# Performance work log

Hardware: AMD Instinct MI355X
Metric: run time of the kernel (lower is better)

The kernel has to match this reference:

```python
import jax, jax.numpy as jnp
import numpy as np

B, T, O, H, CTX, HOR = 32, 24, 128, 512, 256, 48
MAX_STEP = 2.0


def setup_inputs() -> dict:
    key = jax.random.key(0)
    ks = jax.random.split(key, 20)
    def lin(k, out_d, in_d):
        bound = 1.0 / np.sqrt(in_d)
        kw, kb = jax.random.split(k)
        W = jax.random.uniform(kw, (out_d, in_d), jnp.float32, -bound, bound)
        b = jax.random.uniform(kb, (out_d,), jnp.float32, -bound, bound)
        return W, b
    W_emb, b_emb = lin(ks[0], H, 2)
    W_ctx, b_ctx = lin(ks[1], H, CTX)
    Wi_enc, bi_enc = lin(ks[2], 3 * H, H)
    Wh_enc, bh_enc = lin(ks[3], 3 * H, H)
    Wi_cell, bi_cell = lin(ks[4], 3 * H, H)
    Wh_cell, bh_cell = lin(ks[5], 3 * H, H)
    W1, b1 = lin(ks[6], H, H)
    W2, b2 = lin(ks[7], 2, H)
    z_ctx = jax.random.normal(ks[8], (B, CTX), jnp.float32)
    traj_hist = jax.random.uniform(ks[9], (B, T, O, 2), jnp.float32) * 10.0
    return dict(z_ctx=z_ctx, traj_hist=traj_hist,
                W_emb=W_emb, b_emb=b_emb, W_ctx=W_ctx, b_ctx=b_ctx,
                Wi_enc=Wi_enc, Wh_enc=Wh_enc, bi_enc=bi_enc, bh_enc=bh_enc,
                Wi_cell=Wi_cell, Wh_cell=Wh_cell, bi_cell=bi_cell, bh_cell=bh_cell,
                W1=W1, b1=b1, W2=W2, b2=b2, horizon=HOR)


def _gru(h, x, Wi, Wh, bi, bh):
    # PyTorch GRU gate math: gates ordered (r, z, n)
    gi = x @ Wi.T + bi  # [N, 3H]
    gh = h @ Wh.T + bh
    ir, iz, inn = jnp.split(gi, 3, axis=-1)
    hr, hz, hn = jnp.split(gh, 3, axis=-1)
    r = jax.nn.sigmoid(ir + hr)
    z = jax.nn.sigmoid(iz + hz)
    n = jnp.tanh(inn + r * hn)
    return (1.0 - z) * n + z * h


def reference(z_ctx, traj_hist, W_emb, b_emb, W_ctx, b_ctx,
              Wi_enc, Wh_enc, bi_enc, bh_enc,
              Wi_cell, Wh_cell, bi_cell, bh_cell,
              W1, b1, W2, b2, horizon):
    b, t, o, _ = traj_hist.shape
    Hd = W_emb.shape[0]
    seq = traj_hist.transpose(0, 2, 1, 3).reshape(b * o, t, 2)  # [N, t, 2]
    emb = seq @ W_emb.T + b_emb  # [N, t, H]

    h0 = jnp.zeros((b * o, Hd), traj_hist.dtype)
    def enc_step(h, x):
        return _gru(h, x, Wi_enc, Wh_enc, bi_enc, bh_enc), None
    h, _ = jax.lax.scan(enc_step, h0, emb.transpose(1, 0, 2))

    ctx = z_ctx @ W_ctx.T + b_ctx                         # [b, H]
    ctx = jnp.repeat(ctx[:, None, :], o, axis=1).reshape(b * o, Hd)
    h = h + ctx

    state0 = seq[:, -1]  # [N, 2]
    def dec_step(carry, _):
        h, state = carry
        inp = state @ W_emb.T + b_emb
        h = _gru(h, inp, Wi_cell, Wh_cell, bi_cell, bh_cell)
        d = jax.nn.gelu(h @ W1.T + b1, approximate=False) @ W2.T + b2  # [N, 2]
        d = MAX_STEP * jnp.tanh(d / MAX_STEP)
        s = state + d
        state = jnp.stack([jnp.clip(s[..., 0], -90.0, 90.0),
                           jnp.mod(s[..., 1], 360.0)], axis=-1)
        return (h, state), state
    _, outs = jax.lax.scan(dec_step, (h, state0), None, length=horizon)
    # outs: [horizon, N, 2] -> [b, horizon, o, 2]
    return outs.transpose(1, 0, 2).reshape(b, o, horizon, 2).transpose(0, 2, 1, 3)
```

## Files before the change

kernel.cpp:

```cpp
#include <hip/hip_runtime.h>
#include <hip/hip_bf16.h>
#include <math.h>

#define BB 32
#define TT 24
#define OO 128
#define HH 512
#define CTXD 256
#define HOR 48
#define NN (BB*OO)
#define G3 (3*HH)
#define KS2 16
#define TILE_U16 (KS2*512)

typedef unsigned short ushortt;
typedef __attribute__((ext_vector_type(8))) short bf16x8;
typedef __attribute__((ext_vector_type(4))) float f32x4;

__device__ __forceinline__ ushortt f2bf(float x) {
    union { float f; unsigned u; } v; v.f = x;
    unsigned r = v.u + 0x7FFF + ((v.u >> 16) & 1);
    return (ushortt)(r >> 16);
}
__device__ __forceinline__ float bf2f(ushortt b) {
    union { unsigned u; float f; } v; v.u = ((unsigned)b) << 16;
    return v.f;
}
__device__ __forceinline__ void splitbf(float x, ushortt& hi, ushortt& lo) {
    hi = f2bf(x);
    lo = f2bf(x - bf2f(hi));
}
__device__ __forceinline__ float sigm(float x) { return 1.f / (1.f + __expf(-x)); }
__device__ __forceinline__ float tanh_fast(float x) {
    float xc = fminf(fmaxf(x, -10.f), 10.f);
    float e = __expf(2.f * xc);
    return (e - 1.f) / (e + 1.f);
}

__device__ __forceinline__ void group_barrier(unsigned* cnt, unsigned target) {
    __syncthreads();
    if (threadIdx.x == 0) {
        __hip_atomic_fetch_add(cnt, 1u, __ATOMIC_RELAXED, __HIP_MEMORY_SCOPE_AGENT);
        while (__hip_atomic_load(cnt, __ATOMIC_RELAXED, __HIP_MEMORY_SCOPE_AGENT) < target)
            __builtin_amdgcn_s_sleep(2);
    }
    __syncthreads();
    asm volatile("buffer_inv sc0\n\ts_waitcnt vmcnt(0)" ::: "memory");
}


#define MLOADA(Ad, ksv) do { const unsigned ko = (unsigned)(ksv) * 512; \
  _Pragma("unroll") for (int m_ = 0; m_ < 2; m_++) { \
    Ad[m_*2+0] = *reinterpret_cast<const bf16x8*>(RAh + ao[m_] + ko); \
    Ad[m_*2+1] = *reinterpret_cast<const bf16x8*>(RAl + ao[m_] + ko); \
  } } while(0)
#define MLOADB(Bd, ksv) do { const unsigned ko = (unsigned)(ksv) * 512; \
  _Pragma("unroll") for (int i_ = 0; i_ < 6; i_++) { \
    Bd[i_*2+0] = *reinterpret_cast<const bf16x8*>(Bh + bo[i_] + ko); \
    Bd[i_*2+1] = *reinterpret_cast<const bf16x8*>(Bl + bo[i_] + ko); \
  } } while(0)
#define MMFMA(Av, Bv) do { \
  _Pragma("unroll") for (int m_ = 0; m_ < 2; m_++) \
  _Pragma("unroll") for (int i_ = 0; i_ < 6; i_++) \
    acc[m_][i_] = __builtin_amdgcn_mfma_f32_16x16x32_bf16(Av[m_*2+0], Bv[i_*2+0], acc[m_][i_], 0,0,0); \
  _Pragma("unroll") for (int m_ = 0; m_ < 2; m_++) \
  _Pragma("unroll") for (int i_ = 0; i_ < 6; i_++) \
    acc[m_][i_] = __builtin_amdgcn_mfma_f32_16x16x32_bf16(Av[m_*2+0], Bv[i_*2+1], acc[m_][i_], 0,0,0); \
  _Pragma("unroll") for (int m_ = 0; m_ < 2; m_++) \
  _Pragma("unroll") for (int i_ = 0; i_ < 6; i_++) \
    acc[m_][i_] = __builtin_amdgcn_mfma_f32_16x16x32_bf16(Av[m_*2+1], Bv[i_*2+0], acc[m_][i_], 0,0,0); \
  } while(0)

#define HLOADA(Ad, ksv) do { const unsigned ko = (unsigned)(ksv) * 512; \
  _Pragma("unroll") for (int m_ = 0; m_ < 2; m_++) { \
    Ad[m_*2+0] = *reinterpret_cast<const bf16x8*>(WAh + ao[m_] + ko); \
    Ad[m_*2+1] = *reinterpret_cast<const bf16x8*>(WAl + ao[m_] + ko); \
  } } while(0)
#define HLOADB(Bd, ksv) do { const unsigned ko = (unsigned)(ksv) * 512; \
  _Pragma("unroll") for (int n_ = 0; n_ < 2; n_++) { \
    Bd[n_*2+0] = *reinterpret_cast<const bf16x8*>(W1H + bo1[n_] + ko); \
    Bd[n_*2+1] = *reinterpret_cast<const bf16x8*>(W1L + bo1[n_] + ko); \
  } } while(0)
#define HMFMA(Av, Bv) do { \
  _Pragma("unroll") for (int m_ = 0; m_ < 2; m_++) \
  _Pragma("unroll") for (int n_ = 0; n_ < 2; n_++) { \
    hacc[m_][n_] = __builtin_amdgcn_mfma_f32_16x16x32_bf16(Av[m_*2+0], Bv[n_*2+0], hacc[m_][n_], 0,0,0); \
    hacc[m_][n_] = __builtin_amdgcn_mfma_f32_16x16x32_bf16(Av[m_*2+0], Bv[n_*2+1], hacc[m_][n_], 0,0,0); \
    hacc[m_][n_] = __builtin_amdgcn_mfma_f32_16x16x32_bf16(Av[m_*2+1], Bv[n_*2+0], hacc[m_][n_], 0,0,0); \
  } } while(0)

__global__ __launch_bounds__(256, 2) void main_kernel(
    ushortt* Ah0, ushortt* Al0, ushortt* Ah1, ushortt* Al1,
    const ushortt* __restrict__ WheH, const ushortt* __restrict__ WheL,
    const ushortt* __restrict__ WhdH, const ushortt* __restrict__ WhdL,
    const ushortt* __restrict__ W1H,  const ushortt* __restrict__ W1L,
    const float* __restrict__ Ue, const float* __restrict__ ce,
    const float* __restrict__ Ud, const float* __restrict__ cd,
    const float* __restrict__ bhe, const float* __restrict__ bhd,
    const float* __restrict__ traj, const float* __restrict__ ctx,
    const float* __restrict__ b1v, const float* __restrict__ W2,
    const float* __restrict__ b2v, float* __restrict__ dpart,
    unsigned* bar, float* __restrict__ out)
{
    __shared__ float hbuf[128 * 36];
    __shared__ float sstate[128 * 2];
    const int mb = blockIdx.x & 31;
    const int jb = blockIdx.x >> 5;
    const int w = threadIdx.x >> 6, lane = threadIdx.x & 63;
    const int quad = lane >> 4, l15 = lane & 15;
    const int mtg = mb * 8 + w * 2;
    const int jlo = jb * 32;
    unsigned* grpcnt = bar + mb * 16;
    unsigned tgt = 0;

    ushortt* bh_[2] = {Ah0, Ah1};
    ushortt* bl_[2] = {Al0, Al1};

    unsigned ao[2], bo[6], bo1[2];
#pragma unroll
    for (int mt = 0; mt < 2; mt++) ao[mt] = (unsigned)(mtg + mt) * TILE_U16 + lane * 8;
#pragma unroll
    for (int g = 0; g < 3; g++)
#pragma unroll
        for (int jt = 0; jt < 2; jt++)
            bo[g*2+jt] = (unsigned)(g*32 + jb*2 + jt) * TILE_U16 + lane * 8;
#pragma unroll
    for (int nt = 0; nt < 2; nt++) bo1[nt] = (unsigned)(jb*2 + nt) * TILE_U16 + lane * 8;

    float b1r[2], w2a[2], w2b[2];
#pragma unroll
    for (int nt = 0; nt < 2; nt++) {
        int col = jlo + nt*16 + l15;
        b1r[nt] = b1v[col]; w2a[nt] = W2[col]; w2b[nt] = W2[HH + col];
    }
    const float b20 = b2v[0], b21 = b2v[1];

    float Ur0[2],Ur1[2],Uz0[2],Uz1[2],Un0[2],Un1[2],Crr[2],Czz[2],bhn[2],cinn[2];

#pragma unroll 1
    for (int s = 0; s < TT + HOR; s++) {
        const bool enc = s < TT;
        if (s == 0 || s == TT) {
            const float* U  = enc ? Ue : Ud;
            const float* ci = enc ? ce : cd;
            const float* bh = enc ? bhe : bhd;
#pragma unroll
            for (int jt = 0; jt < 2; jt++) {
                int j = jlo + jt*16 + l15;
                Ur0[jt] = U[j*2];            Ur1[jt] = U[j*2+1];
                Uz0[jt] = U[(512+j)*2];      Uz1[jt] = U[(512+j)*2+1];
                Un0[jt] = U[(1024+j)*2];     Un1[jt] = U[(1024+j)*2+1];
                Crr[jt] = ci[j] + bh[j];
                Czz[jt] = ci[512+j] + bh[512+j];
                cinn[jt] = ci[1024+j];       bhn[jt] = bh[1024+j];
            }
            if (!enc) {
                if (threadIdx.x < 128) {
                    int lrow = threadIdx.x;
                    const float* sp = traj + (((size_t)mb * TT + 23) * OO + lrow) * 2;
                    sstate[lrow*2] = sp[0]; sstate[lrow*2+1] = sp[1];
                }
                __syncthreads();
            }
        }
        const ushortt* RAh = bh_[s & 1];
        const ushortt* RAl = bl_[s & 1];
        ushortt* WAh = bh_[(s + 1) & 1];
        ushortt* WAl = bl_[(s + 1) & 1];
        const ushortt* Bh = enc ? WheH : WhdH;
        const ushortt* Bl = enc ? WheL : WhdL;

        f32x4 acc[2][6];
#pragma unroll
        for (int a = 0; a < 2; a++)
#pragma unroll
            for (int b = 0; b < 6; b++) acc[a][b] = (f32x4){0.f,0.f,0.f,0.f};

        if (s > 0) {
            bf16x8 aC[4], bC[12], aN[4], bN[12];
            MLOADA(aC, 0); MLOADB(bC, 0);
#pragma unroll 1
            for (int ks = 0; ks < 14; ks += 2) {
                MLOADA(aN, ks+1); MLOADB(bN, ks+1);
                MMFMA(aC, bC);
                MLOADA(aC, ks+2); MLOADB(bC, ks+2);
                MMFMA(aN, bN);
            }
            MLOADA(aN, 15); MLOADB(bN, 15);
            MMFMA(aC, bC);
            MMFMA(aN, bN);
        }

        float x0v[2][4], x1v[2][4];
#pragma unroll
        for (int mt = 0; mt < 2; mt++)
#pragma unroll
            for (int reg = 0; reg < 4; reg++) {
                int lrow = (w*2 + mt) * 16 + quad * 4 + reg;
                if (enc) {
                    const float* p = traj + (((size_t)mb * TT + s) * OO + lrow) * 2;
                    x0v[mt][reg] = p[0]; x1v[mt][reg] = p[1];
                } else {
                    x0v[mt][reg] = sstate[lrow*2]; x1v[mt][reg] = sstate[lrow*2+1];
                }
            }

#pragma unroll
        for (int mt = 0; mt < 2; mt++)
#pragma unroll
            for (int jt = 0; jt < 2; jt++) {
                int qk = jt*2 + (l15 >> 3), slot = l15 & 7;
#pragma unroll
                for (int reg = 0; reg < 4; reg++) {
                    float x0 = x0v[mt][reg], x1 = x1v[mt][reg];
                    float pr = acc[mt][0+jt][reg] + fmaf(x1, Ur1[jt], fmaf(x0, Ur0[jt], Crr[jt]));
                    float pz = acc[mt][2+jt][reg] + fmaf(x1, Uz1[jt], fmaf(x0, Uz0[jt], Czz[jt]));
                    float hn = acc[mt][4+jt][reg] + bhn[jt];
                    float inn = fmaf(x1, Un1[jt], fmaf(x0, Un0[jt], cinn[jt]));
                    float hold = 0.f;
                    if (s > 0) {
                        unsigned pos = (unsigned)(mtg + mt) * TILE_U16 + (unsigned)jb * 512
                                     + (unsigned)(qk*16 + quad*4 + reg) * 8 + slot;
                        hold = bf2f(RAh[pos]) + bf2f(RAl[pos]);
                    }
                    float rg = sigm(pr), zg = sigm(pz);
                    float nn = tanh_fast(inn + rg * hn);
                    float h = (1.f - zg) * nn + zg * hold;
                    if (enc && s == TT - 1)
                        h += ctx[(size_t)mb * HH + jlo + jt*16 + l15];
                    hbuf[(w*32 + mt*16 + quad*4 + reg) * 36 + jt*16 + l15] = h;
                }
            }
        __syncthreads();
#pragma unroll
        for (int rr = 0; rr < 2; rr++) {
            int fr = threadIdx.x + 256 * rr;
            int mt8 = fr >> 6, fl = fr & 63;
            int qk = fl >> 4, rloc = mt8 * 16 + (fl & 15);
            const float4 v0 = *reinterpret_cast<const float4*>(&hbuf[rloc * 36 + qk * 8]);
            const float4 v1 = *reinterpret_cast<const float4*>(&hbuf[rloc * 36 + qk * 8 + 4]);
            float src[8] = {v0.x, v0.y, v0.z, v0.w, v1.x, v1.y, v1.z, v1.w};
            bf16x8 hv, lv;
#pragma unroll
            for (int q = 0; q < 8; q++) {
                ushortt hi, lo; splitbf(src[q], hi, lo);
                hv[q] = (short)hi; lv[q] = (short)lo;
            }
            unsigned base = (unsigned)(mb*8 + mt8) * TILE_U16 + (unsigned)jb * 512 + fl * 8;
            *reinterpret_cast<bf16x8*>(WAh + base) = hv;
            *reinterpret_cast<bf16x8*>(WAl + base) = lv;
        }
        __syncthreads();

        tgt += 16;
        group_barrier(grpcnt, tgt);

        if (!enc) {
            f32x4 hacc[2][2];
#pragma unroll
            for (int a = 0; a < 2; a++)
#pragma unroll
                for (int b = 0; b < 2; b++) hacc[a][b] = (f32x4){0.f,0.f,0.f,0.f};
            {
                bf16x8 aC[4], bC[4], aN[4], bN[4];
                HLOADA(aC, 0); HLOADB(bC, 0);
#pragma unroll 1
                for (int ks = 0; ks < 14; ks += 2) {
                    HLOADA(aN, ks+1); HLOADB(bN, ks+1);
                    HMFMA(aC, bC);
                    HLOADA(aC, ks+2); HLOADB(bC, ks+2);
                    HMFMA(aN, bN);
                }
                HLOADA(aN, 15); HLOADB(bN, 15);
                HMFMA(aC, bC);
                HMFMA(aN, bN);
            }
            float p0[2][4], p1[2][4];
#pragma unroll
            for (int mt = 0; mt < 2; mt++)
#pragma unroll
                for (int reg = 0; reg < 4; reg++) { p0[mt][reg] = 0.f; p1[mt][reg] = 0.f; }
#pragma unroll
            for (int mt = 0; mt < 2; mt++)
#pragma unroll
                for (int nt = 0; nt < 2; nt++)
#pragma unroll
                    for (int reg = 0; reg < 4; reg++) {
                        float v = hacc[mt][nt][reg] + b1r[nt];
                        v = 0.5f * v * (1.0f + erff(v * 0.70710678118654752440f));
                        p0[mt][reg] = fmaf(v, w2a[nt], p0[mt][reg]);
                        p1[mt][reg] = fmaf(v, w2b[nt], p1[mt][reg]);
                    }
#pragma unroll
            for (int m = 1; m < 16; m <<= 1)
#pragma unroll
                for (int mt = 0; mt < 2; mt++)
#pragma unroll
                    for (int reg = 0; reg < 4; reg++) {
                        p0[mt][reg] += __shfl_xor(p0[mt][reg], m, 64);
                        p1[mt][reg] += __shfl_xor(p1[mt][reg], m, 64);
                    }
            if (l15 == 0) {
#pragma unroll
                for (int mt = 0; mt < 2; mt++)
#pragma unroll
                    for (int reg = 0; reg < 4; reg++) {
                        int lrow = (w*2 + mt) * 16 + quad * 4 + reg;
                        float* dp = dpart + ((size_t)(mb*16 + jb) * 128 + lrow) * 2;
                        dp[0] = p0[mt][reg]; dp[1] = p1[mt][reg];
                    }
            }
            tgt += 16;
            group_barrier(grpcnt, tgt);
            if (threadIdx.x < 128) {
                int lrow = threadIdx.x;
                float d0 = 0.f, d1 = 0.f;
#pragma unroll
                for (int j2 = 0; j2 < 16; j2++) {
                    const float* dp = dpart + ((size_t)(mb*16 + j2) * 128 + lrow) * 2;
                    d0 += dp[0]; d1 += dp[1];
                }
                d0 += b20; d1 += b21;
                d0 = 2.0f * tanhf(d0 * 0.5f);
                d1 = 2.0f * tanhf(d1 * 0.5f);
                float s0 = sstate[lrow*2] + d0;
                s0 = fminf(fmaxf(s0, -90.f), 90.f);
                float s1 = sstate[lrow*2+1] + d1;
                float rrm = fmodf(s1, 360.f);
                if (rrm < 0.f) rrm += 360.f;
                sstate[lrow*2] = s0; sstate[lrow*2+1] = rrm;
                if (jb == 0) {
                    float* op = out + (((size_t)mb * HOR + (s - TT)) * OO + lrow) * 2;
                    op[0] = s0; op[1] = rrm;
                }
            }
            __syncthreads();
        }
    }
}

__device__ __forceinline__ void pack16(const float* __restrict__ W,
                                       ushortt* __restrict__ Fh, ushortt* __restrict__ Fl,
                                       int item) {
    int n = item >> 6, rem = item & 63;
    int ks = rem >> 2, quadk = rem & 3;
    int nt = n >> 4, l15 = n & 15;
    ushortt hv[8], lv[8];
#pragma unroll
    for (int q = 0; q < 8; q++) {
        float v = W[(size_t)n * 512 + ks*32 + quadk*8 + q];
        ushortt hi, lo; splitbf(v, hi, lo);
        hv[q] = hi; lv[q] = lo;
    }
    size_t pos = ((size_t)nt * TILE_U16) + (size_t)ks * 512 + (quadk*16 + l15) * 8;
#pragma unroll
    for (int q = 0; q < 8; q++) { Fh[pos + q] = hv[q]; Fl[pos + q] = lv[q]; }
}

__global__ __launch_bounds__(256) void prep_kernel(
    const float* __restrict__ Wh_enc, const float* __restrict__ Wh_cell,
    const float* __restrict__ W1,
    const float* __restrict__ Wi_enc, const float* __restrict__ bi_enc,
    const float* __restrict__ Wi_cell, const float* __restrict__ bi_cell,
    const float* __restrict__ W_emb, const float* __restrict__ b_emb,
    const float* __restrict__ z, const float* __restrict__ Wc, const float* __restrict__ bc,
    ushortt* __restrict__ WheH, ushortt* __restrict__ WheL,
    ushortt* __restrict__ WhdH, ushortt* __restrict__ WhdL,
    ushortt* __restrict__ W1H, ushortt* __restrict__ W1L,
    float* __restrict__ Ue, float* __restrict__ ce,
    float* __restrict__ Ud, float* __restrict__ cd,
    float* __restrict__ ctx, unsigned* __restrict__ bar)
{
    int b = blockIdx.x;
    if (b < 384) {
        pack16(Wh_enc, WheH, WheL, b * 256 + threadIdx.x);
    } else if (b < 768) {
        pack16(Wh_cell, WhdH, WhdL, (b - 384) * 256 + threadIdx.x);
    } else if (b < 896) {
        pack16(W1, W1H, W1L, (b - 768) * 256 + threadIdx.x);
    } else if (b < 1664) {
        int w = threadIdx.x >> 6, lane = threadIdx.x & 63;
        int gidx = (b - 896) * 4 + w;
        int which = gidx >= G3;
        int j = gidx - which * G3;
        const float* Wi = which ? Wi_cell : Wi_enc;
        const float* bi = which ? bi_cell : bi_enc;
        float u0 = 0.f, u1 = 0.f, cc = 0.f;
#pragma unroll
        for (int i = 0; i < 8; i++) {
            int k = i * 64 + lane;
            float wv = Wi[(size_t)j * HH + k];
            u0 = fmaf(wv, W_emb[2*k],   u0);
            u1 = fmaf(wv, W_emb[2*k+1], u1);
            cc = fmaf(wv, b_emb[k],     cc);
        }
#pragma unroll
        for (int m = 1; m < 64; m <<= 1) {
            u0 += __shfl_xor(u0, m, 64);
            u1 += __shfl_xor(u1, m, 64);
            cc += __shfl_xor(cc, m, 64);
        }
        if (lane == 0) {
            float* Uo = which ? Ud : Ue;
            float* cv = which ? cd : ce;
            Uo[j*2] = u0; Uo[j*2+1] = u1; cv[j] = cc + bi[j];
        }
    } else if (b < 1728) {
        int idx = (b - 1664) * 256 + threadIdx.x;
        int bb = idx >> 9, j = idx & 511;
        float acc = bc[j];
        const float4* zp = (const float4*)(z + (size_t)bb * CTXD);
        const float4* wp = (const float4*)(Wc + (size_t)j * CTXD);
#pragma unroll 4
        for (int k = 0; k < CTXD / 4; k++) {
            float4 a = zp[k], ww = wp[k];
            acc = fmaf(a.x, ww.x, fmaf(a.y, ww.y, fmaf(a.z, ww.z, fmaf(a.w, ww.w, acc))));
        }
        ctx[idx] = acc;
    } else {
        bar[threadIdx.x] = 0u;
        bar[threadIdx.x + 256] = 0u;
    }
}

extern "C" void kernel_launch(void* const* d_in, const int* in_sizes, int n_in,
                              void* d_out, int out_size, void* d_ws, size_t ws_size,
                              hipStream_t stream) {
    const float* z_ctx   = (const float*)d_in[0];
    const float* traj    = (const float*)d_in[1];
    const float* W_emb   = (const float*)d_in[2];
    const float* b_emb   = (const float*)d_in[3];
    const float* W_ctx   = (const float*)d_in[4];
    const float* b_ctx   = (const float*)d_in[5];
    const float* Wi_enc  = (const float*)d_in[6];
    const float* Wh_enc  = (const float*)d_in[7];
    const float* bi_enc  = (const float*)d_in[8];
    const float* bh_enc  = (const float*)d_in[9];
    const float* Wi_cell = (const float*)d_in[10];
    const float* Wh_cell = (const float*)d_in[11];
    const float* bi_cell = (const float*)d_in[12];
    const float* bh_cell = (const float*)d_in[13];
    const float* W1      = (const float*)d_in[14];
    const float* b1      = (const float*)d_in[15];
    const float* W2      = (const float*)d_in[16];
    const float* b2      = (const float*)d_in[17];
    float* out = (float*)d_out;

    char* ws = (char*)d_ws;
    size_t off = 0;
    auto alloc = [&](size_t bytes) { void* p = ws + off; off += (bytes + 255) & ~(size_t)255; return p; };
    const size_t hfrag  = (size_t)256 * TILE_U16 * 2;
    const size_t wfrag  = (size_t)96  * TILE_U16 * 2;
    const size_t w1frag = (size_t)32  * TILE_U16 * 2;
    ushortt* Ah0 = (ushortt*)alloc(hfrag);
    ushortt* Al0 = (ushortt*)alloc(hfrag);
    ushortt* Ah1 = (ushortt*)alloc(hfrag);
    ushortt* Al1 = (ushortt*)alloc(hfrag);
    ushortt* WheH = (ushortt*)alloc(wfrag);
    ushortt* WheL = (ushortt*)alloc(wfrag);
    ushortt* WhdH = (ushortt*)alloc(wfrag);
    ushortt* WhdL = (ushortt*)alloc(wfrag);
    ushortt* W1H  = (ushortt*)alloc(w1frag);
    ushortt* W1L  = (ushortt*)alloc(w1frag);
    float*   Ue   = (float*)alloc((size_t)G3 * 2 * 4);
    float*   ce   = (float*)alloc((size_t)G3 * 4);
    float*   Ud   = (float*)alloc((size_t)G3 * 2 * 4);
    float*   cd   = (float*)alloc((size_t)G3 * 4);
    float*   ctxb = (float*)alloc((size_t)BB * HH * 4);
    float*   dpart = (float*)alloc((size_t)32 * 16 * 128 * 2 * 4);
    unsigned* bar  = (unsigned*)alloc(512 * 4);

    prep_kernel<<<1729, 256, 0, stream>>>(Wh_enc, Wh_cell, W1,
                                          Wi_enc, bi_enc, Wi_cell, bi_cell,
                                          W_emb, b_emb, z_ctx, W_ctx, b_ctx,
                                          WheH, WheL, WhdH, WhdL, W1H, W1L,
                                          Ue, ce, Ud, cd, ctxb, bar);

    main_kernel<<<512, 256, 0, stream>>>(Ah0, Al0, Ah1, Al1,
                                         WheH, WheL, WhdH, WhdL, W1H, W1L,
                                         Ue, ce, Ud, cd, bh_enc, bh_cell,
                                         traj, ctxb, b1, W2, b2,
                                         dpart, bar, out);
}
```

Before: 3.498 ms.

## Split hidden columns across twice as many blocks and keep old h in LDS

Each block now owns 16 hidden columns instead of 32, and the grid doubles to 1024 blocks with launch bounds raised to 4 blocks per CU. The per-block accumulators, B-fragment loads and W1 tiles shrink to match, and the partial sums for the output head are spread over 32 slices instead of 16. The previous hidden value is now read from the block's own LDS buffer rather than reloaded from the global split-bf16 buffers, and one __syncthreads before the group barrier is dropped. The aim is more parallelism and occupancy per step, at the price of a grid barrier that needs twice as many arrivals and more redundant A-operand loads across blocks.

```diff
diff --git a/kernel.cpp b/kernel.cpp
--- a/kernel.cpp
+++ b/kernel.cpp
@@ -55,20 +55,20 @@
     Ad[m_*2+1] = *reinterpret_cast<const bf16x8*>(RAl + ao[m_] + ko); \
   } } while(0)
 #define MLOADB(Bd, ksv) do { const unsigned ko = (unsigned)(ksv) * 512; \
-  _Pragma("unroll") for (int i_ = 0; i_ < 6; i_++) { \
-    Bd[i_*2+0] = *reinterpret_cast<const bf16x8*>(Bh + bo[i_] + ko); \
-    Bd[i_*2+1] = *reinterpret_cast<const bf16x8*>(Bl + bo[i_] + ko); \
+  _Pragma("unroll") for (int g_ = 0; g_ < 3; g_++) { \
+    Bd[g_*2+0] = *reinterpret_cast<const bf16x8*>(Bh + bo[g_] + ko); \
+    Bd[g_*2+1] = *reinterpret_cast<const bf16x8*>(Bl + bo[g_] + ko); \
   } } while(0)
 #define MMFMA(Av, Bv) do { \
   _Pragma("unroll") for (int m_ = 0; m_ < 2; m_++) \
-  _Pragma("unroll") for (int i_ = 0; i_ < 6; i_++) \
-    acc[m_][i_] = __builtin_amdgcn_mfma_f32_16x16x32_bf16(Av[m_*2+0], Bv[i_*2+0], acc[m_][i_], 0,0,0); \
+  _Pragma("unroll") for (int g_ = 0; g_ < 3; g_++) \
+    acc[m_][g_] = __builtin_amdgcn_mfma_f32_16x16x32_bf16(Av[m_*2+0], Bv[g_*2+0], acc[m_][g_], 0,0,0); \
   _Pragma("unroll") for (int m_ = 0; m_ < 2; m_++) \
-  _Pragma("unroll") for (int i_ = 0; i_ < 6; i_++) \
-    acc[m_][i_] = __builtin_amdgcn_mfma_f32_16x16x32_bf16(Av[m_*2+0], Bv[i_*2+1], acc[m_][i_], 0,0,0); \
+  _Pragma("unroll") for (int g_ = 0; g_ < 3; g_++) \
+    acc[m_][g_] = __builtin_amdgcn_mfma_f32_16x16x32_bf16(Av[m_*2+0], Bv[g_*2+1], acc[m_][g_], 0,0,0); \
   _Pragma("unroll") for (int m_ = 0; m_ < 2; m_++) \
-  _Pragma("unroll") for (int i_ = 0; i_ < 6; i_++) \
-    acc[m_][i_] = __builtin_amdgcn_mfma_f32_16x16x32_bf16(Av[m_*2+1], Bv[i_*2+0], acc[m_][i_], 0,0,0); \
+  _Pragma("unroll") for (int g_ = 0; g_ < 3; g_++) \
+    acc[m_][g_] = __builtin_amdgcn_mfma_f32_16x16x32_bf16(Av[m_*2+1], Bv[g_*2+0], acc[m_][g_], 0,0,0); \
   } while(0)
 
 #define HLOADA(Ad, ksv) do { const unsigned ko = (unsigned)(ksv) * 512; \
@@ -77,19 +77,17 @@
     Ad[m_*2+1] = *reinterpret_cast<const bf16x8*>(WAl + ao[m_] + ko); \
   } } while(0)
 #define HLOADB(Bd, ksv) do { const unsigned ko = (unsigned)(ksv) * 512; \
-  _Pragma("unroll") for (int n_ = 0; n_ < 2; n_++) { \
-    Bd[n_*2+0] = *reinterpret_cast<const bf16x8*>(W1H + bo1[n_] + ko); \
-    Bd[n_*2+1] = *reinterpret_cast<const bf16x8*>(W1L + bo1[n_] + ko); \
+    Bd[0] = *reinterpret_cast<const bf16x8*>(W1H + bo1 + ko); \
+    Bd[1] = *reinterpret_cast<const bf16x8*>(W1L + bo1 + ko); \
+  } while(0)
+#define HMFMA(Av, Bv) do { \
+  _Pragma("unroll") for (int m_ = 0; m_ < 2; m_++) { \
+    hacc[m_] = __builtin_amdgcn_mfma_f32_16x16x32_bf16(Av[m_*2+0], Bv[0], hacc[m_], 0,0,0); \
+    hacc[m_] = __builtin_amdgcn_mfma_f32_16x16x32_bf16(Av[m_*2+0], Bv[1], hacc[m_], 0,0,0); \
+    hacc[m_] = __builtin_amdgcn_mfma_f32_16x16x32_bf16(Av[m_*2+1], Bv[0], hacc[m_], 0,0,0); \
   } } while(0)
-#define HMFMA(Av, Bv) do { \
-  _Pragma("unroll") for (int m_ = 0; m_ < 2; m_++) \
-  _Pragma("unroll") for (int n_ = 0; n_ < 2; n_++) { \
-    hacc[m_][n_] = __builtin_amdgcn_mfma_f32_16x16x32_bf16(Av[m_*2+0], Bv[n_*2+0], hacc[m_][n_], 0,0,0); \
-    hacc[m_][n_] = __builtin_amdgcn_mfma_f32_16x16x32_bf16(Av[m_*2+0], Bv[n_*2+1], hacc[m_][n_], 0,0,0); \
-    hacc[m_][n_] = __builtin_amdgcn_mfma_f32_16x16x32_bf16(Av[m_*2+1], Bv[n_*2+0], hacc[m_][n_], 0,0,0); \
-  } } while(0)
-
-__global__ __launch_bounds__(256, 2) void main_kernel(
+
+__global__ __launch_bounds__(256, 4) void main_kernel(
     ushortt* Ah0, ushortt* Al0, ushortt* Ah1, ushortt* Al1,
     const ushortt* __restrict__ WheH, const ushortt* __restrict__ WheL,
     const ushortt* __restrict__ WhdH, const ushortt* __restrict__ WhdL,
@@ -102,40 +100,32 @@
     const float* __restrict__ b2v, float* __restrict__ dpart,
     unsigned* bar, float* __restrict__ out)
 {
-    __shared__ float hbuf[128 * 36];
+    __shared__ float hbuf[128 * 20];
     __shared__ float sstate[128 * 2];
     const int mb = blockIdx.x & 31;
     const int jb = blockIdx.x >> 5;
     const int w = threadIdx.x >> 6, lane = threadIdx.x & 63;
     const int quad = lane >> 4, l15 = lane & 15;
     const int mtg = mb * 8 + w * 2;
-    const int jlo = jb * 32;
+    const int jlo = jb * 16;
+    const int jcol = jlo + l15;
     unsigned* grpcnt = bar + mb * 16;
     unsigned tgt = 0;
 
     ushortt* bh_[2] = {Ah0, Ah1};
     ushortt* bl_[2] = {Al0, Al1};
 
-    unsigned ao[2], bo[6], bo1[2];
+    unsigned ao[2], bo[3], bo1;
 #pragma unroll
     for (int mt = 0; mt < 2; mt++) ao[mt] = (unsigned)(mtg + mt) * TILE_U16 + lane * 8;
 #pragma unroll
-    for (int g = 0; g < 3; g++)
-#pragma unroll
-        for (int jt = 0; jt < 2; jt++)
-            bo[g*2+jt] = (unsigned)(g*32 + jb*2 + jt) * TILE_U16 + lane * 8;
-#pragma unroll
-    for (int nt = 0; nt < 2; nt++) bo1[nt] = (unsigned)(jb*2 + nt) * TILE_U16 + lane * 8;
-
-    float b1r[2], w2a[2], w2b[2];
-#pragma unroll
-    for (int nt = 0; nt < 2; nt++) {
-        int col = jlo + nt*16 + l15;
-        b1r[nt] = b1v[col]; w2a[nt] = W2[col]; w2b[nt] = W2[HH + col];
-    }
+    for (int g = 0; g < 3; g++) bo[g] = (unsigned)(g*32 + jb) * TILE_U16 + lane * 8;
+    bo1 = (unsigned)jb * TILE_U16 + lane * 8;
+
+    const float b1r = b1v[jcol], w2a = W2[jcol], w2b = W2[HH + jcol];
     const float b20 = b2v[0], b21 = b2v[1];
 
-    float Ur0[2],Ur1[2],Uz0[2],Uz1[2],Un0[2],Un1[2],Crr[2],Czz[2],bhn[2],cinn[2];
+    float Ur0, Ur1, Uz0, Uz1, Un0, Un1, Crr, Czz, bhn, cinn;
 
 #pragma unroll 1
     for (int s = 0; s < TT + HOR; s++) {
@@ -144,16 +134,12 @@
             const float* U  = enc ? Ue : Ud;
             const float* ci = enc ? ce : cd;
             const float* bh = enc ? bhe : bhd;
-#pragma unroll
-            for (int jt = 0; jt < 2; jt++) {
-                int j = jlo + jt*16 + l15;
-                Ur0[jt] = U[j*2];            Ur1[jt] = U[j*2+1];
-                Uz0[jt] = U[(512+j)*2];      Uz1[jt] = U[(512+j)*2+1];
-                Un0[jt] = U[(1024+j)*2];     Un1[jt] = U[(1024+j)*2+1];
-                Crr[jt] = ci[j] + bh[j];
-                Czz[jt] = ci[512+j] + bh[512+j];
-                cinn[jt] = ci[1024+j];       bhn[jt] = bh[1024+j];
-            }
+            Ur0 = U[jcol*2];            Ur1 = U[jcol*2+1];
+            Uz0 = U[(512+jcol)*2];      Uz1 = U[(512+jcol)*2+1];
+            Un0 = U[(1024+jcol)*2];     Un1 = U[(1024+jcol)*2+1];
+            Crr = ci[jcol] + bh[jcol];
+            Czz = ci[512+jcol] + bh[512+jcol];
+            cinn = ci[1024+jcol];       bhn = bh[1024+jcol];
             if (!enc) {
                 if (threadIdx.x < 128) {
                     int lrow = threadIdx.x;
@@ -170,14 +156,14 @@
         const ushortt* Bh = enc ? WheH : WhdH;
         const ushortt* Bl = enc ? WheL : WhdL;
 
-        f32x4 acc[2][6];
+        f32x4 acc[2][3];
 #pragma unroll
         for (int a = 0; a < 2; a++)
 #pragma unroll
-            for (int b = 0; b < 6; b++) acc[a][b] = (f32x4){0.f,0.f,0.f,0.f};
+            for (int g = 0; g < 3; g++) acc[a][g] = (f32x4){0.f,0.f,0.f,0.f};
 
         if (s > 0) {
-            bf16x8 aC[4], bC[12], aN[4], bN[12];
+            bf16x8 aC[4], bC[6], aN[4], bN[6];
             MLOADA(aC, 0); MLOADB(bC, 0);
 #pragma unroll 1
             for (int ks = 0; ks < 14; ks += 2) {
@@ -208,37 +194,28 @@
 #pragma unroll
         for (int mt = 0; mt < 2; mt++)
 #pragma unroll
-            for (int jt = 0; jt < 2; jt++) {
-                int qk = jt*2 + (l15 >> 3), slot = l15 & 7;
-#pragma unroll
-                for (int reg = 0; reg < 4; reg++) {
-                    float x0 = x0v[mt][reg], x1 = x1v[mt][reg];
-                    float pr = acc[mt][0+jt][reg] + fmaf(x1, Ur1[jt], fmaf(x0, Ur0[jt], Crr[jt]));
-                    float pz = acc[mt][2+jt][reg] + fmaf(x1, Uz1[jt], fmaf(x0, Uz0[jt], Czz[jt]));
-                    float hn = acc[mt][4+jt][reg] + bhn[jt];
-                    float inn = fmaf(x1, Un1[jt], fmaf(x0, Un0[jt], cinn[jt]));
-                    float hold = 0.f;
-                    if (s > 0) {
-                        unsigned pos = (unsigned)(mtg + mt) * TILE_U16 + (unsigned)jb * 512
-                                     + (unsigned)(qk*16 + quad*4 + reg) * 8 + slot;
-                        hold = bf2f(RAh[pos]) + bf2f(RAl[pos]);
-                    }
-                    float rg = sigm(pr), zg = sigm(pz);
-                    float nn = tanh_fast(inn + rg * hn);
-                    float h = (1.f - zg) * nn + zg * hold;
-                    if (enc && s == TT - 1)
-                        h += ctx[(size_t)mb * HH + jlo + jt*16 + l15];
-                    hbuf[(w*32 + mt*16 + quad*4 + reg) * 36 + jt*16 + l15] = h;
-                }
+            for (int reg = 0; reg < 4; reg++) {
+                int lrow = (w*2 + mt) * 16 + quad * 4 + reg;
+                float x0 = x0v[mt][reg], x1 = x1v[mt][reg];
+                float pr = acc[mt][0][reg] + fmaf(x1, Ur1, fmaf(x0, Ur0, Crr));
+                float pz = acc[mt][1][reg] + fmaf(x1, Uz1, fmaf(x0, Uz0, Czz));
+                float hn = acc[mt][2][reg] + bhn;
+                float inn = fmaf(x1, Un1, fmaf(x0, Un0, cinn));
+                float hold = (s > 0) ? hbuf[lrow * 20 + l15] : 0.f;
+                float rg = sigm(pr), zg = sigm(pz);
+                float nn = tanh_fast(inn + rg * hn);
+                float h = (1.f - zg) * nn + zg * hold;
+                if (enc && s == TT - 1)
+                    h += ctx[(size_t)mb * HH + jcol];
+                hbuf[lrow * 20 + l15] = h;
             }
         __syncthreads();
-#pragma unroll
-        for (int rr = 0; rr < 2; rr++) {
-            int fr = threadIdx.x + 256 * rr;
-            int mt8 = fr >> 6, fl = fr & 63;
-            int qk = fl >> 4, rloc = mt8 * 16 + (fl & 15);
-            const float4 v0 = *reinterpret_cast<const float4*>(&hbuf[rloc * 36 + qk * 8]);
-            const float4 v1 = *reinterpret_cast<const float4*>(&hbuf[rloc * 36 + qk * 8 + 4]);
+        {
+            int fr = threadIdx.x;
+            int mt8 = fr >> 5, rem = fr & 31;
+            int qk = rem >> 4, r15 = rem & 15;
+            const float4 v0 = *reinterpret_cast<const float4*>(&hbuf[(mt8*16 + r15) * 20 + qk * 8]);
+            const float4 v1 = *reinterpret_cast<const float4*>(&hbuf[(mt8*16 + r15) * 20 + qk * 8 + 4]);
             float src[8] = {v0.x, v0.y, v0.z, v0.w, v1.x, v1.y, v1.z, v1.w};
             bf16x8 hv, lv;
 #pragma unroll
@@ -246,23 +223,22 @@
                 ushortt hi, lo; splitbf(src[q], hi, lo);
                 hv[q] = (short)hi; lv[q] = (short)lo;
             }
-            unsigned base = (unsigned)(mb*8 + mt8) * TILE_U16 + (unsigned)jb * 512 + fl * 8;
+            int quadg = (jb & 1) * 2 + qk;
+            unsigned base = (unsigned)(mb*8 + mt8) * TILE_U16 + (unsigned)(jb >> 1) * 512
+                          + (unsigned)(quadg * 16 + r15) * 8;
             *reinterpret_cast<bf16x8*>(WAh + base) = hv;
             *reinterpret_cast<bf16x8*>(WAl + base) = lv;
         }
-        __syncthreads();
-
-        tgt += 16;
+
+        tgt += 32;
         group_barrier(grpcnt, tgt);
 
         if (!enc) {
-            f32x4 hacc[2][2];
-#pragma unroll
-            for (int a = 0; a < 2; a++)
-#pragma unroll
-                for (int b = 0; b < 2; b++) hacc[a][b] = (f32x4){0.f,0.f,0.f,0.f};
+            f32x4 hacc[2];
+            hacc[0] = (f32x4){0.f,0.f,0.f,0.f};
+            hacc[1] = (f32x4){0.f,0.f,0.f,0.f};
             {
-                bf16x8 aC[4], bC[4], aN[4], bN[4];
+                bf16x8 aC[4], bC[2], aN[4], bN[2];
                 HLOADA(aC, 0); HLOADB(bC, 0);
 #pragma unroll 1
                 for (int ks = 0; ks < 14; ks += 2) {
@@ -279,18 +255,12 @@
 #pragma unroll
             for (int mt = 0; mt < 2; mt++)
 #pragma unroll
-                for (int reg = 0; reg < 4; reg++) { p0[mt][reg] = 0.f; p1[mt][reg] = 0.f; }
-#pragma unroll
-            for (int mt = 0; mt < 2; mt++)
-#pragma unroll
-                for (int nt = 0; nt < 2; nt++)
-#pragma unroll
-                    for (int reg = 0; reg < 4; reg++) {
-                        float v = hacc[mt][nt][reg] + b1r[nt];
-                        v = 0.5f * v * (1.0f + erff(v * 0.70710678118654752440f));
-                        p0[mt][reg] = fmaf(v, w2a[nt], p0[mt][reg]);
-                        p1[mt][reg] = fmaf(v, w2b[nt], p1[mt][reg]);
-                    }
+                for (int reg = 0; reg < 4; reg++) {
+                    float v = hacc[mt][reg] + b1r;
+                    v = 0.5f * v * (1.0f + erff(v * 0.70710678118654752440f));
+                    p0[mt][reg] = v * w2a;
+                    p1[mt][reg] = v * w2b;
+                }
 #pragma unroll
             for (int m = 1; m < 16; m <<= 1)
 #pragma unroll
@@ -306,18 +276,18 @@
 #pragma unroll
                     for (int reg = 0; reg < 4; reg++) {
                         int lrow = (w*2 + mt) * 16 + quad * 4 + reg;
-                        float* dp = dpart + ((size_t)(mb*16 + jb) * 128 + lrow) * 2;
+                        float* dp = dpart + ((size_t)(mb*32 + jb) * 128 + lrow) * 2;
                         dp[0] = p0[mt][reg]; dp[1] = p1[mt][reg];
                     }
             }
-            tgt += 16;
+            tgt += 32;
             group_barrier(grpcnt, tgt);
             if (threadIdx.x < 128) {
                 int lrow = threadIdx.x;
                 float d0 = 0.f, d1 = 0.f;
-#pragma unroll
-                for (int j2 = 0; j2 < 16; j2++) {
-                    const float* dp = dpart + ((size_t)(mb*16 + j2) * 128 + lrow) * 2;
+#pragma unroll 8
+                for (int j2 = 0; j2 < 32; j2++) {
+                    const float* dp = dpart + ((size_t)(mb*32 + j2) * 128 + lrow) * 2;
                     d0 += dp[0]; d1 += dp[1];
                 }
                 d0 += b20; d1 += b21;
@@ -462,13 +432,13 @@
     ushortt* WhdL = (ushortt*)alloc(wfrag);
     ushortt* W1H  = (ushortt*)alloc(w1frag);
     ushortt* W1L  = (ushortt*)alloc(w1frag);
-    float*   Ue   = (float*)alloc((size_t)G3 * 2 * 4);
-    float*   ce   = (float*)alloc((size_t)G3 * 4);
-    float*   Ud   = (float*)alloc((size_t)G3 * 2 * 4);
-    float*   cd   = (float*)alloc((size_t)G3 * 4);
-    float*   ctxb = (float*)alloc((size_t)BB * HH * 4);
-    float*   dpart = (float*)alloc((size_t)32 * 16 * 128 * 2 * 4);
-    unsigned* bar  = (unsigned*)alloc(512 * 4);
+    float* Ue   = (float*)alloc((size_t)G3 * 2 * 4);
+    float* ce   = (float*)alloc((size_t)G3 * 4);
+    float* Ud   = (float*)alloc((size_t)G3 * 2 * 4);
+    float* cd   = (float*)alloc((size_t)G3 * 4);
+    float* ctxb = (float*)alloc((size_t)BB * HH * 4);
+    float* dpart = (float*)alloc((size_t)32 * 32 * 128 * 2 * 4);
+    unsigned* bar = (unsigned*)alloc(512 * 4);
 
     prep_kernel<<<1729, 256, 0, stream>>>(Wh_enc, Wh_cell, W1,
                                           Wi_enc, bi_enc, Wi_cell, bi_cell,
@@ -476,9 +446,9 @@
                                           WheH, WheL, WhdH, WhdL, W1H, W1L,
                                           Ue, ce, Ud, cd, ctxb, bar);
 
-    main_kernel<<<512, 256, 0, stream>>>(Ah0, Al0, Ah1, Al1,
-                                         WheH, WheL, WhdH, WhdL, W1H, W1L,
-                                         Ue, ce, Ud, cd, bh_enc, bh_cell,
-                                         traj, ctxb, b1, W2, b2,
-                                         dpart, bar, out);
-}
+    main_kernel<<<1024, 256, 0, stream>>>(Ah0, Al0, Ah1, Al1,
+                                          WheH, WheL, WhdH, WhdL, W1H, W1L,
+                                          Ue, ce, Ud, cd, bh_enc, bh_cell,
+                                          traj, ctxb, b1, W2, b2,
+                                          dpart, bar, out);
+}
```

Measured after the change: 4.205 ms. 1.2x slower.
